# Kernel optimization log

Measured on AMD Instinct MI355X. Metric: run time of the kernel, lower is better.

Reference implementation:

```python
import jax, jax.numpy as jnp
import numpy as np

N = 100000
E = 1600000
EPS = 1e-5

def setup_inputs() -> dict:
    key = jax.random.key(0)
    ks = jax.random.split(key, 10)
    d_in, d_h, d_out = 128, 128, 64
    sc = lambda d: 1.0 / np.sqrt(d)
    return {
        "x": jax.random.normal(ks[0], (N, d_in), jnp.float32),
        "edge_src": jax.random.randint(ks[1], (E,), 0, N, jnp.int32),
        "edge_dst": jax.random.randint(ks[2], (E,), 0, N, jnp.int32),
        "Wr0": jax.random.normal(ks[3], (d_in, d_h), jnp.float32) * sc(d_in),
        "Wn0": jax.random.normal(ks[4], (d_in, d_h), jnp.float32) * sc(d_in),
        "b0": jnp.zeros((d_h,), jnp.float32),
        "g0": jnp.ones((d_h,), jnp.float32),
        "be0": jnp.zeros((d_h,), jnp.float32),
        "Wr1": jax.random.normal(ks[5], (d_h, d_h), jnp.float32) * sc(d_h),
        "Wn1": jax.random.normal(ks[6], (d_h, d_h), jnp.float32) * sc(d_h),
        "b1": jnp.zeros((d_h,), jnp.float32),
        "g1": jnp.ones((d_h,), jnp.float32),
        "be1": jnp.zeros((d_h,), jnp.float32),
        "Wr2": jax.random.normal(ks[7], (d_h, d_out), jnp.float32) * sc(d_h),
        "Wn2": jax.random.normal(ks[8], (d_h, d_out), jnp.float32) * sc(d_h),
        "b2": jnp.zeros((d_out,), jnp.float32),
    }

def _mean_agg(x, src, dst):
    # GraphSAGE mean aggregation: scatter-mean of source features onto dst nodes
    deg = jax.ops.segment_sum(jnp.ones((src.shape[0],), x.dtype), dst, num_segments=N)
    s = jax.ops.segment_sum(x[src], dst, num_segments=N)  # [N, d] gather+scatter
    return s / jnp.maximum(deg, 1.0)[:, None]

def _sage_conv(x, src, dst, Wr, Wn, b):
    return x @ Wr + _mean_agg(x, src, dst) @ Wn + b

def _layernorm(h, g, b):
    mu = h.mean(-1, keepdims=True)
    var = ((h - mu) ** 2).mean(-1, keepdims=True)
    return (h - mu) * jax.lax.rsqrt(var + EPS) * g + b

def reference(x, edge_src, edge_dst, Wr0, Wn0, b0, g0, be0,
              Wr1, Wn1, b1, g1, be1, Wr2, Wn2, b2):
    # layer 0: conv -> dropout(eval=identity) -> LayerNorm -> relu
    h = _sage_conv(x, edge_src, edge_dst, Wr0, Wn0, b0)
    h = jax.nn.relu(_layernorm(h, g0, be0))
    # layer 1
    h = _sage_conv(h, edge_src, edge_dst, Wr1, Wn1, b1)
    h = jax.nn.relu(_layernorm(h, g1, be1))
    # final conv + log_softmax over classes
    h = _sage_conv(h, edge_src, edge_dst, Wr2, Wn2, b2)
    return jax.nn.log_softmax(h, axis=1)
```

## Files before the change

kernel.cpp:

```cpp
#include <hip/hip_runtime.h>
#include <math.h>

#define N_NODES 100000
#define NPAD 100032
#define N_EDGES 1600000
#define EPS 1e-5f
#define NC 256
#define CHUNK 6250
#define NR 98
#define RSZ 1024
#define NRC (NR * NC)

typedef __bf16 bf16x8 __attribute__((ext_vector_type(8)));
typedef float f32x4 __attribute__((ext_vector_type(4)));
typedef float f32x2 __attribute__((ext_vector_type(2)));

__device__ inline unsigned short f2bf(float f) {
    unsigned u = __float_as_uint(f);
    unsigned r = u + 0x7fffu + ((u >> 16) & 1u);
    return (unsigned short)(r >> 16);
}
__device__ inline float bflo(unsigned u) { return __uint_as_float(u << 16); }
__device__ inline float bfhi(unsigned u) { return __uint_as_float(u & 0xffff0000u); }
__device__ inline unsigned pack2(float lo, float hi) {
    return (unsigned)f2bf(lo) | ((unsigned)f2bf(hi) << 16);
}
__device__ inline unsigned char f2fp8(float f) {
    return (unsigned char)(__builtin_amdgcn_cvt_pk_fp8_f32(f, f, 0, false) & 0xff);
}

__global__ __launch_bounds__(256) void k_prep(const float* __restrict__ x,
                                              unsigned short* __restrict__ xb,
                                              unsigned* __restrict__ xq8,
                                              const int* __restrict__ dst,
                                              int* __restrict__ cntG) {
    __shared__ int hist[NR];
    int t = threadIdx.x;
    if (blockIdx.x < 12500) {
        int idx = blockIdx.x * 256 + t;
        float4 v = ((const float4*)x)[idx];
        ushort4 o;
        o.x = f2bf(v.x); o.y = f2bf(v.y); o.z = f2bf(v.z); o.w = f2bf(v.w);
        ((ushort4*)xb)[idx] = o;
        int q = __builtin_amdgcn_cvt_pk_fp8_f32(v.x, v.y, 0, false);
        q = __builtin_amdgcn_cvt_pk_fp8_f32(v.z, v.w, q, true);
        xq8[idx] = (unsigned)q;
    } else {
        int c = blockIdx.x - 12500;
        for (int i = t; i < NR; i += 256) hist[i] = 0;
        __syncthreads();
        int base = c * CHUNK;
        for (int i = base + t; i < base + CHUNK; i += 256)
            atomicAdd(&hist[dst[i] >> 10], 1);
        __syncthreads();
        for (int i = t; i < NR; i += 256) cntG[i * NC + c] = hist[i];
    }
}

__global__ __launch_bounds__(256) void k_scanA_prepw(
        int* __restrict__ cntG,
        const float* __restrict__ Wr0, const float* __restrict__ Wn0,
        const float* __restrict__ Wr1, const float* __restrict__ Wn1,
        const float* __restrict__ Wr2, const float* __restrict__ Wn2,
        unsigned short* __restrict__ WT0, unsigned short* __restrict__ WT1,
        unsigned short* __restrict__ WT2) {
    int t = threadIdx.x;
    if (blockIdx.x == 0) {
        __shared__ int ts[256];
        const int PER = NRC / 256;
        int s = 0;
        for (int i = 0; i < PER; ++i) s += cntG[t * PER + i];
        ts[t] = s;
        __syncthreads();
        #pragma unroll
        for (int off = 1; off < 256; off <<= 1) {
            int y = 0;
            if (t >= off) y = ts[t - off];
            __syncthreads();
            if (t >= off) ts[t] += y;
            __syncthreads();
        }
        int run = ts[t] - s;
        for (int i = 0; i < PER; ++i) {
            int v = cntG[t * PER + i];
            cntG[t * PER + i] = run;
            run += v;
        }
    } else {
        int b = blockIdx.x - 1;
        if (b < 256) {
            const float* Wr = (b < 128) ? Wr0 : Wr1;
            const float* Wn = (b < 128) ? Wn0 : Wn1;
            unsigned short* WT = (b < 128) ? WT0 : WT1;
            int idx = (b & 127) * 256 + t;
            int n = idx >> 8;
            int kc = idx & 255;
            float v = (kc < 128) ? Wr[kc * 128 + n] : Wn[(kc - 128) * 128 + n];
            WT[idx] = f2bf(v);
        } else {
            int idx = (b - 256) * 256 + t;
            int n = idx >> 7;
            int k = idx & 127;
            float v = (n < 64) ? Wr2[k * 64 + n] : Wn2[k * 64 + (n - 64)];
            WT2[n * 128 + k] = f2bf(v);
        }
    }
}

__global__ __launch_bounds__(1024) void k_bin(const int* __restrict__ src,
                                              const int* __restrict__ dst,
                                              const int* __restrict__ baseG,
                                              unsigned* __restrict__ bpack) {
    __shared__ int cur[NR];
    int t = threadIdx.x, c = blockIdx.x;
    for (int i = t; i < NR; i += 1024) cur[i] = baseG[i * NC + c];
    __syncthreads();
    int base = c * CHUNK;
    for (int i = base + t; i < base + CHUNK; i += 1024) {
        int d = dst[i];
        unsigned s = (unsigned)src[i];
        int p = atomicAdd(&cur[d >> 10], 1);
        bpack[p] = (s << 10) | (unsigned)(d & 1023);
    }
}

__global__ __launch_bounds__(1024) void k_nodeplace(
        const unsigned* __restrict__ bpack, const int* __restrict__ baseG,
        int* __restrict__ deg, float* __restrict__ invdeg,
        int* __restrict__ rowptr, int* __restrict__ eidx) {
    __shared__ int hist[RSZ];
    __shared__ int cur[RSZ];
    __shared__ int wbase[16];
    int r = blockIdx.x, t = threadIdx.x;
    hist[t] = 0;
    __syncthreads();
    int s0 = baseG[r * NC];
    int s1 = (r == NR - 1) ? N_EDGES : baseG[(r + 1) * NC];
    int nbase = r << 10;
    for (int i = s0 + t; i < s1; i += 1024)
        atomicAdd(&hist[bpack[i] & 1023u], 1);
    __syncthreads();
    int lane = t & 63, wv = t >> 6;
    int d = hist[t];
    int s = d;
    #pragma unroll
    for (int m = 1; m < 64; m <<= 1) {
        int y = __shfl_up(s, m);
        if (lane >= m) s += y;
    }
    if (lane == 63) wbase[wv] = s;
    __syncthreads();
    if (t < 16) {
        int v = wbase[t];
        int sv = v;
        #pragma unroll
        for (int m = 1; m < 16; m <<= 1) {
            int y = __shfl_up(sv, m);
            if (t >= m) sv += y;
        }
        wbase[t] = sv - v;
    }
    __syncthreads();
    int p = s0 + wbase[wv] + s - d;
    cur[t] = p;
    int n = nbase + t;
    if (n < N_NODES) {
        rowptr[n] = p;
        deg[n] = d;
        invdeg[n] = 1.0f / fmaxf((float)d, 1.0f);
    }
    __syncthreads();
    for (int i = s0 + t; i < s1; i += 1024) {
        unsigned bp = bpack[i];
        int pp = atomicAdd(&cur[bp & 1023u], 1);
        eidx[pp] = (int)(bp >> 10);
    }
}

__global__ __launch_bounds__(256) void k_gather(const uint4* __restrict__ hq4,
                                                const int* __restrict__ eidx,
                                                const int* __restrict__ rowptr,
                                                const int* __restrict__ deg,
                                                const float* __restrict__ invdeg,
                                                uint4* __restrict__ aggw4) {
    int node = blockIdx.x * 32 + (threadIdx.x >> 3);
    int l = threadIdx.x & 7;
    int start = rowptr[node];
    int cnt = deg[node];
    f32x2 a[8];
    #pragma unroll
    for (int i = 0; i < 8; ++i) a[i] = (f32x2)0.0f;

    auto accum = [&](uint4 u) {
        a[0] += __builtin_amdgcn_cvt_pk_f32_fp8((int)u.x, false);
        a[1] += __builtin_amdgcn_cvt_pk_f32_fp8((int)u.x, true);
        a[2] += __builtin_amdgcn_cvt_pk_f32_fp8((int)u.y, false);
        a[3] += __builtin_amdgcn_cvt_pk_f32_fp8((int)u.y, true);
        a[4] += __builtin_amdgcn_cvt_pk_f32_fp8((int)u.z, false);
        a[5] += __builtin_amdgcn_cvt_pk_f32_fp8((int)u.z, true);
        a[6] += __builtin_amdgcn_cvt_pk_f32_fp8((int)u.w, false);
        a[7] += __builtin_amdgcn_cvt_pk_f32_fp8((int)u.w, true);
    };

    int j = 0;
    for (; j + 4 <= cnt; j += 4) {
        int s0 = eidx[start + j];
        int s1 = eidx[start + j + 1];
        int s2 = eidx[start + j + 2];
        int s3 = eidx[start + j + 3];
        uint4 u0 = hq4[(size_t)s0 * 8 + l];
        uint4 u1 = hq4[(size_t)s1 * 8 + l];
        uint4 u2 = hq4[(size_t)s2 * 8 + l];
        uint4 u3 = hq4[(size_t)s3 * 8 + l];
        accum(u0); accum(u1); accum(u2); accum(u3);
    }
    for (; j < cnt; ++j) {
        uint4 u = hq4[(size_t)eidx[start + j] * 8 + l];
        accum(u);
    }

    float id = invdeg[node];
    uint4 o0, o1;
    o0.x = pack2(a[0].x * id, a[0].y * id);
    o0.y = pack2(a[1].x * id, a[1].y * id);
    o0.z = pack2(a[2].x * id, a[2].y * id);
    o0.w = pack2(a[3].x * id, a[3].y * id);
    o1.x = pack2(a[4].x * id, a[4].y * id);
    o1.y = pack2(a[5].x * id, a[5].y * id);
    o1.z = pack2(a[6].x * id, a[6].y * id);
    o1.w = pack2(a[7].x * id, a[7].y * id);
    aggw4[(size_t)node * 16 + l * 2] = o0;
    aggw4[(size_t)node * 16 + l * 2 + 1] = o1;
}

__global__ __launch_bounds__(512) void k_gemm_ln(
        const unsigned short* __restrict__ hb, const unsigned short* __restrict__ ab,
        const unsigned short* __restrict__ WT,
        const float* __restrict__ b, const float* __restrict__ g,
        const float* __restrict__ be, unsigned short* __restrict__ outb,
        unsigned char* __restrict__ outq8) {
    __shared__ unsigned short hl[64][136];
    __shared__ unsigned short al[64][136];
    __shared__ unsigned short bt[128][72];
    __shared__ float p1[2][64], p2[2][64];

    const int tid = threadIdx.x;
    const int lane = tid & 63;
    const int w = tid >> 6;
    const int quad = lane >> 4;
    const int l15 = lane & 15;
    const int rt = w >> 1;
    const int ch = w & 1;
    const int row0 = blockIdx.x * 64;

    #pragma unroll
    for (int t = 0; t < 2; ++t) {
        int idx = tid + t * 512;
        int r = idx >> 4;
        int c8 = idx & 15;
        *(float4*)&hl[r][c8 * 8] = ((const float4*)hb)[(size_t)(row0 + r) * 16 + c8];
        *(float4*)&al[r][c8 * 8] = ((const float4*)ab)[(size_t)(row0 + r) * 16 + c8];
    }

    f32x4 acc[4];
    #pragma unroll
    for (int t = 0; t < 4; ++t)
        #pragma unroll
        for (int r = 0; r < 4; ++r) acc[t][r] = 0.0f;

    #pragma unroll
    for (int kt = 0; kt < 4; ++kt) {
        __syncthreads();
        #pragma unroll
        for (int t = 0; t < 2; ++t) {
            int idx = tid + t * 512;
            int n = idx >> 3;
            int c8 = idx & 7;
            *(float4*)&bt[n][c8 * 8] = ((const float4*)WT)[n * 32 + kt * 8 + c8];
        }
        __syncthreads();
        #pragma unroll
        for (int ks = 0; ks < 2; ++ks) {
            const int ck = kt * 64 + ks * 32;
            const unsigned short* ap = (ck < 128)
                ? &hl[rt * 16 + l15][ck + quad * 8]
                : &al[rt * 16 + l15][ck - 128 + quad * 8];
            bf16x8 a = *(const bf16x8*)ap;
            #pragma unroll
            for (int t = 0; t < 4; ++t) {
                bf16x8 bb = *(const bf16x8*)&bt[ch * 64 + t * 16 + l15][ks * 32 + quad * 8];
                acc[t] = __builtin_amdgcn_mfma_f32_16x16x32_bf16(a, bb, acc[t], 0, 0, 0);
            }
        }
    }

    float bcol[4], gc[4], bec[4];
    #pragma unroll
    for (int t = 0; t < 4; ++t) {
        int col = ch * 64 + t * 16 + l15;
        bcol[t] = b[col]; gc[t] = g[col]; bec[t] = be[col];
    }
    float v[4][4];
    float s1[4], s2[4];
    #pragma unroll
    for (int r = 0; r < 4; ++r) { s1[r] = 0.0f; s2[r] = 0.0f; }
    #pragma unroll
    for (int t = 0; t < 4; ++t)
        #pragma unroll
        for (int r = 0; r < 4; ++r) {
            float x = acc[t][r] + bcol[t];
            v[t][r] = x;
            s1[r] += x;
            s2[r] += x * x;
        }
    #pragma unroll
    for (int m = 1; m <= 8; m <<= 1)
        #pragma unroll
        for (int r = 0; r < 4; ++r) {
            s1[r] += __shfl_xor(s1[r], m);
            s2[r] += __shfl_xor(s2[r], m);
        }
    if (l15 == 0) {
        #pragma unroll
        for (int r = 0; r < 4; ++r) {
            int rl = rt * 16 + quad * 4 + r;
            p1[ch][rl] = s1[r];
            p2[ch][rl] = s2[r];
        }
    }
    __syncthreads();
    #pragma unroll
    for (int r = 0; r < 4; ++r) {
        int rl = rt * 16 + quad * 4 + r;
        float S1 = p1[0][rl] + p1[1][rl];
        float S2 = p2[0][rl] + p2[1][rl];
        float mean = S1 * (1.0f / 128.0f);
        float var = S2 * (1.0f / 128.0f) - mean * mean;
        float rstd = rsqrtf(var + EPS);
        #pragma unroll
        for (int t = 0; t < 4; ++t) {
            int col = ch * 64 + t * 16 + l15;
            float o = fmaxf((v[t][r] - mean) * rstd * gc[t] + bec[t], 0.0f);
            outb[(size_t)(row0 + rl) * 128 + col] = f2bf(o);
            if (outq8) outq8[(size_t)(row0 + rl) * 128 + col] = f2fp8(o);
        }
    }
}

__global__ __launch_bounds__(512) void k_gemm2(
        const unsigned short* __restrict__ hb, const unsigned short* __restrict__ WT,
        const float* __restrict__ b2, unsigned short* __restrict__ zb16,
        unsigned char* __restrict__ yq8) {
    __shared__ unsigned short hl[64][136];
    __shared__ unsigned short bt[128][136];

    const int tid = threadIdx.x;
    const int lane = tid & 63;
    const int w = tid >> 6;
    const int quad = lane >> 4;
    const int l15 = lane & 15;
    const int rt = w >> 1;
    const int ch = w & 1;
    const int row0 = blockIdx.x * 64;

    #pragma unroll
    for (int t = 0; t < 2; ++t) {
        int idx = tid + t * 512;
        int r = idx >> 4;
        int c8 = idx & 15;
        *(float4*)&hl[r][c8 * 8] = ((const float4*)hb)[(size_t)(row0 + r) * 16 + c8];
    }
    #pragma unroll
    for (int t = 0; t < 4; ++t) {
        int idx = tid + t * 512;
        int n = idx >> 4;
        int c8 = idx & 15;
        *(float4*)&bt[n][c8 * 8] = ((const float4*)WT)[n * 16 + c8];
    }
    __syncthreads();

    f32x4 acc[4];
    #pragma unroll
    for (int t = 0; t < 4; ++t)
        #pragma unroll
        for (int r = 0; r < 4; ++r) acc[t][r] = 0.0f;

    #pragma unroll
    for (int ks = 0; ks < 4; ++ks) {
        bf16x8 a = *(const bf16x8*)&hl[rt * 16 + l15][ks * 32 + quad * 8];
        #pragma unroll
        for (int t = 0; t < 4; ++t) {
            bf16x8 bb = *(const bf16x8*)&bt[ch * 64 + t * 16 + l15][ks * 32 + quad * 8];
            acc[t] = __builtin_amdgcn_mfma_f32_16x16x32_bf16(a, bb, acc[t], 0, 0, 0);
        }
    }

    if (ch == 0) {
        #pragma unroll
        for (int t = 0; t < 4; ++t) {
            int col = t * 16 + l15;
            float bc = b2[col];
            #pragma unroll
            for (int r = 0; r < 4; ++r) {
                int rl = rt * 16 + quad * 4 + r;
                zb16[(size_t)(row0 + rl) * 64 + col] = f2bf(acc[t][r] + bc);
            }
        }
    } else {
        #pragma unroll
        for (int t = 0; t < 4; ++t) {
            int col = t * 16 + l15;
            #pragma unroll
            for (int r = 0; r < 4; ++r) {
                int rl = rt * 16 + quad * 4 + r;
                yq8[(size_t)(row0 + rl) * 64 + col] = f2fp8(acc[t][r]);
            }
        }
    }
}

__global__ __launch_bounds__(256) void k_l2g(const uint4* __restrict__ yq4,
                                             const unsigned short* __restrict__ zb16,
                                             const int* __restrict__ eidx,
                                             const int* __restrict__ rowptr,
                                             const int* __restrict__ deg,
                                             const float* __restrict__ invdeg,
                                             float* __restrict__ out) {
    int node = blockIdx.x * 64 + (threadIdx.x >> 2);
    if (node >= N_NODES) return;
    int l = threadIdx.x & 3;
    int start = rowptr[node];
    int cnt = deg[node];
    f32x2 a[8];
    #pragma unroll
    for (int i = 0; i < 8; ++i) a[i] = (f32x2)0.0f;

    auto accum = [&](uint4 u) {
        a[0] += __builtin_amdgcn_cvt_pk_f32_fp8((int)u.x, false);
        a[1] += __builtin_amdgcn_cvt_pk_f32_fp8((int)u.x, true);
        a[2] += __builtin_amdgcn_cvt_pk_f32_fp8((int)u.y, false);
        a[3] += __builtin_amdgcn_cvt_pk_f32_fp8((int)u.y, true);
        a[4] += __builtin_amdgcn_cvt_pk_f32_fp8((int)u.z, false);
        a[5] += __builtin_amdgcn_cvt_pk_f32_fp8((int)u.z, true);
        a[6] += __builtin_amdgcn_cvt_pk_f32_fp8((int)u.w, false);
        a[7] += __builtin_amdgcn_cvt_pk_f32_fp8((int)u.w, true);
    };

    int j = 0;
    for (; j + 4 <= cnt; j += 4) {
        int s0 = eidx[start + j];
        int s1 = eidx[start + j + 1];
        int s2 = eidx[start + j + 2];
        int s3 = eidx[start + j + 3];
        uint4 u0 = yq4[(size_t)s0 * 4 + l];
        uint4 u1 = yq4[(size_t)s1 * 4 + l];
        uint4 u2 = yq4[(size_t)s2 * 4 + l];
        uint4 u3 = yq4[(size_t)s3 * 4 + l];
        accum(u0); accum(u1); accum(u2); accum(u3);
    }
    for (; j < cnt; ++j) {
        uint4 u = yq4[(size_t)eidx[start + j] * 4 + l];
        accum(u);
    }

    float id = invdeg[node];
    uint4 z0 = ((const uint4*)zb16)[(size_t)node * 8 + l * 2];
    uint4 z1 = ((const uint4*)zb16)[(size_t)node * 8 + l * 2 + 1];
    float v[16];
    v[0]  = bflo(z0.x) + a[0].x * id; v[1]  = bfhi(z0.x) + a[0].y * id;
    v[2]  = bflo(z0.y) + a[1].x * id; v[3]  = bfhi(z0.y) + a[1].y * id;
    v[4]  = bflo(z0.z) + a[2].x * id; v[5]  = bfhi(z0.z) + a[2].y * id;
    v[6]  = bflo(z0.w) + a[3].x * id; v[7]  = bfhi(z0.w) + a[3].y * id;
    v[8]  = bflo(z1.x) + a[4].x * id; v[9]  = bfhi(z1.x) + a[4].y * id;
    v[10] = bflo(z1.y) + a[5].x * id; v[11] = bfhi(z1.y) + a[5].y * id;
    v[12] = bflo(z1.z) + a[6].x * id; v[13] = bfhi(z1.z) + a[6].y * id;
    v[14] = bflo(z1.w) + a[7].x * id; v[15] = bfhi(z1.w) + a[7].y * id;

    float m = v[0];
    #pragma unroll
    for (int i = 1; i < 16; ++i) m = fmaxf(m, v[i]);
    m = fmaxf(m, __shfl_xor(m, 1));
    m = fmaxf(m, __shfl_xor(m, 2));
    float s = 0.0f;
    #pragma unroll
    for (int i = 0; i < 16; ++i) s += __expf(v[i] - m);
    s += __shfl_xor(s, 1);
    s += __shfl_xor(s, 2);
    float L = m + logf(s);
    #pragma unroll
    for (int k = 0; k < 4; ++k) {
        float4 o;
        o.x = v[4 * k] - L; o.y = v[4 * k + 1] - L;
        o.z = v[4 * k + 2] - L; o.w = v[4 * k + 3] - L;
        ((float4*)out)[(size_t)node * 16 + l * 4 + k] = o;
    }
}

extern "C" void kernel_launch(void* const* d_in, const int* in_sizes, int n_in,
                              void* d_out, int out_size, void* d_ws, size_t ws_size,
                              hipStream_t stream) {
    const float* x   = (const float*)d_in[0];
    const int* esrc  = (const int*)d_in[1];
    const int* edst  = (const int*)d_in[2];
    const float* Wr0 = (const float*)d_in[3];
    const float* Wn0 = (const float*)d_in[4];
    const float* b0  = (const float*)d_in[5];
    const float* g0  = (const float*)d_in[6];
    const float* be0 = (const float*)d_in[7];
    const float* Wr1 = (const float*)d_in[8];
    const float* Wn1 = (const float*)d_in[9];
    const float* b1  = (const float*)d_in[10];
    const float* g1  = (const float*)d_in[11];
    const float* be1 = (const float*)d_in[12];
    const float* Wr2 = (const float*)d_in[13];
    const float* Wn2 = (const float*)d_in[14];
    const float* b2  = (const float*)d_in[15];
    float* out = (float*)d_out;

    char* p = (char*)d_ws;
    auto alloc = [&](size_t bytes) {
        void* r = (void*)p;
        p += (bytes + 255) & ~(size_t)255;
        return r;
    };
    int*   deg    = (int*)  alloc(N_NODES * 4);
    float* invdeg = (float*)alloc(N_NODES * 4);
    int*   rowptr = (int*)  alloc(N_NODES * 4);
    int*   cntG   = (int*)  alloc(NRC * 4);
    unsigned* bpack = (unsigned*)alloc((size_t)N_EDGES * 4);
    int*   eidx   = (int*)  alloc((size_t)N_EDGES * 4);
    unsigned short* xb   = (unsigned short*)alloc((size_t)NPAD * 128 * 2);
    unsigned short* h1   = (unsigned short*)alloc((size_t)NPAD * 128 * 2);
    unsigned short* aggb = (unsigned short*)alloc((size_t)NPAD * 128 * 2);
    unsigned*       xq8  = (unsigned*)      alloc((size_t)N_NODES * 128);
    unsigned char*  h1q8 = (unsigned char*) alloc((size_t)NPAD * 128);
    unsigned short* zb16 = (unsigned short*)alloc((size_t)NPAD * 64 * 2);
    unsigned char*  yq8  = (unsigned char*) alloc((size_t)NPAD * 64);
    unsigned short* WT0  = (unsigned short*)alloc(128 * 256 * 2);
    unsigned short* WT1  = (unsigned short*)alloc(128 * 256 * 2);
    unsigned short* WT2  = (unsigned short*)alloc(128 * 128 * 2);

    k_prep<<<12500 + NC, 256, 0, stream>>>(x, xb, xq8, edst, cntG);
    k_scanA_prepw<<<321, 256, 0, stream>>>(cntG, Wr0, Wn0, Wr1, Wn1, Wr2, Wn2,
                                           WT0, WT1, WT2);
    k_bin<<<NC, 1024, 0, stream>>>(esrc, edst, cntG, bpack);
    k_nodeplace<<<NR, 1024, 0, stream>>>(bpack, cntG, deg, invdeg, rowptr, eidx);

    k_gather<<<N_NODES / 32, 256, 0, stream>>>((const uint4*)xq8, eidx, rowptr, deg, invdeg, (uint4*)aggb);
    k_gemm_ln<<<NPAD / 64, 512, 0, stream>>>(xb, aggb, WT0, b0, g0, be0, h1, h1q8);

    k_gather<<<N_NODES / 32, 256, 0, stream>>>((const uint4*)h1q8, eidx, rowptr, deg, invdeg, (uint4*)aggb);
    k_gemm_ln<<<NPAD / 64, 512, 0, stream>>>(h1, aggb, WT1, b1, g1, be1, xb, (unsigned char*)nullptr);

    k_gemm2<<<NPAD / 64, 512, 0, stream>>>(xb, WT2, b2, zb16, yq8);
    k_l2g<<<(N_NODES + 63) / 64, 256, 0, stream>>>((const uint4*)yq8, zb16, eidx, rowptr, deg, invdeg, out);
}
```

Baseline: 353.4 us.

## Fuse neighbor mean-gather into the GEMM+LayerNorm kernel prologue

Removes the separate k_gather kernel and computes each 64-row tile's mean-aggregated neighbor features directly into shared memory inside k_gemm_ln. This drops the bf16 aggregation buffer's write and read round trip through global memory, plus two kernel launches. In exchange the GEMM blocks must wait on irregular gather latency before doing any math. The launch bounds now request higher occupancy (512 threads, 4 blocks), which may limit registers.

```diff
diff --git a/kernel.cpp b/kernel.cpp
--- a/kernel.cpp
+++ b/kernel.cpp
@@ -177,64 +177,11 @@
     }
 }
 
-__global__ __launch_bounds__(256) void k_gather(const uint4* __restrict__ hq4,
-                                                const int* __restrict__ eidx,
-                                                const int* __restrict__ rowptr,
-                                                const int* __restrict__ deg,
-                                                const float* __restrict__ invdeg,
-                                                uint4* __restrict__ aggw4) {
-    int node = blockIdx.x * 32 + (threadIdx.x >> 3);
-    int l = threadIdx.x & 7;
-    int start = rowptr[node];
-    int cnt = deg[node];
-    f32x2 a[8];
-    #pragma unroll
-    for (int i = 0; i < 8; ++i) a[i] = (f32x2)0.0f;
-
-    auto accum = [&](uint4 u) {
-        a[0] += __builtin_amdgcn_cvt_pk_f32_fp8((int)u.x, false);
-        a[1] += __builtin_amdgcn_cvt_pk_f32_fp8((int)u.x, true);
-        a[2] += __builtin_amdgcn_cvt_pk_f32_fp8((int)u.y, false);
-        a[3] += __builtin_amdgcn_cvt_pk_f32_fp8((int)u.y, true);
-        a[4] += __builtin_amdgcn_cvt_pk_f32_fp8((int)u.z, false);
-        a[5] += __builtin_amdgcn_cvt_pk_f32_fp8((int)u.z, true);
-        a[6] += __builtin_amdgcn_cvt_pk_f32_fp8((int)u.w, false);
-        a[7] += __builtin_amdgcn_cvt_pk_f32_fp8((int)u.w, true);
-    };
-
-    int j = 0;
-    for (; j + 4 <= cnt; j += 4) {
-        int s0 = eidx[start + j];
-        int s1 = eidx[start + j + 1];
-        int s2 = eidx[start + j + 2];
-        int s3 = eidx[start + j + 3];
-        uint4 u0 = hq4[(size_t)s0 * 8 + l];
-        uint4 u1 = hq4[(size_t)s1 * 8 + l];
-        uint4 u2 = hq4[(size_t)s2 * 8 + l];
-        uint4 u3 = hq4[(size_t)s3 * 8 + l];
-        accum(u0); accum(u1); accum(u2); accum(u3);
-    }
-    for (; j < cnt; ++j) {
-        uint4 u = hq4[(size_t)eidx[start + j] * 8 + l];
-        accum(u);
-    }
-
-    float id = invdeg[node];
-    uint4 o0, o1;
-    o0.x = pack2(a[0].x * id, a[0].y * id);
-    o0.y = pack2(a[1].x * id, a[1].y * id);
-    o0.z = pack2(a[2].x * id, a[2].y * id);
-    o0.w = pack2(a[3].x * id, a[3].y * id);
-    o1.x = pack2(a[4].x * id, a[4].y * id);
-    o1.y = pack2(a[5].x * id, a[5].y * id);
-    o1.z = pack2(a[6].x * id, a[6].y * id);
-    o1.w = pack2(a[7].x * id, a[7].y * id);
-    aggw4[(size_t)node * 16 + l * 2] = o0;
-    aggw4[(size_t)node * 16 + l * 2 + 1] = o1;
-}
-
-__global__ __launch_bounds__(512) void k_gemm_ln(
-        const unsigned short* __restrict__ hb, const unsigned short* __restrict__ ab,
+__global__ __launch_bounds__(512, 4) void k_gemm_ln(
+        const unsigned short* __restrict__ hb,
+        const uint4* __restrict__ hq4,
+        const int* __restrict__ eidx, const int* __restrict__ rowptr,
+        const int* __restrict__ deg, const float* __restrict__ invdeg,
         const unsigned short* __restrict__ WT,
         const float* __restrict__ b, const float* __restrict__ g,
         const float* __restrict__ be, unsigned short* __restrict__ outb,
@@ -259,7 +206,57 @@
         int r = idx >> 4;
         int c8 = idx & 15;
         *(float4*)&hl[r][c8 * 8] = ((const float4*)hb)[(size_t)(row0 + r) * 16 + c8];
-        *(float4*)&al[r][c8 * 8] = ((const float4*)ab)[(size_t)(row0 + r) * 16 + c8];
+    }
+
+    {
+        int r = tid >> 3;
+        int l = tid & 7;
+        int node = row0 + r;
+        uint4 o0 = {0, 0, 0, 0}, o1 = {0, 0, 0, 0};
+        if (node < N_NODES) {
+            int start = rowptr[node];
+            int cnt = deg[node];
+            f32x2 a[8];
+            #pragma unroll
+            for (int i = 0; i < 8; ++i) a[i] = (f32x2)0.0f;
+            auto accum = [&](uint4 u) {
+                a[0] += __builtin_amdgcn_cvt_pk_f32_fp8((int)u.x, false);
+                a[1] += __builtin_amdgcn_cvt_pk_f32_fp8((int)u.x, true);
+                a[2] += __builtin_amdgcn_cvt_pk_f32_fp8((int)u.y, false);
+                a[3] += __builtin_amdgcn_cvt_pk_f32_fp8((int)u.y, true);
+                a[4] += __builtin_amdgcn_cvt_pk_f32_fp8((int)u.z, false);
+                a[5] += __builtin_amdgcn_cvt_pk_f32_fp8((int)u.z, true);
+                a[6] += __builtin_amdgcn_cvt_pk_f32_fp8((int)u.w, false);
+                a[7] += __builtin_amdgcn_cvt_pk_f32_fp8((int)u.w, true);
+            };
+            int j = 0;
+            for (; j + 4 <= cnt; j += 4) {
+                int s0 = eidx[start + j];
+                int s1 = eidx[start + j + 1];
+                int s2 = eidx[start + j + 2];
+                int s3 = eidx[start + j + 3];
+                uint4 u0 = hq4[(size_t)s0 * 8 + l];
+                uint4 u1 = hq4[(size_t)s1 * 8 + l];
+                uint4 u2 = hq4[(size_t)s2 * 8 + l];
+                uint4 u3 = hq4[(size_t)s3 * 8 + l];
+                accum(u0); accum(u1); accum(u2); accum(u3);
+            }
+            for (; j < cnt; ++j) {
+                uint4 u = hq4[(size_t)eidx[start + j] * 8 + l];
+                accum(u);
+            }
+            float id = invdeg[node];
+            o0.x = pack2(a[0].x * id, a[0].y * id);
+            o0.y = pack2(a[1].x * id, a[1].y * id);
+            o0.z = pack2(a[2].x * id, a[2].y * id);
+            o0.w = pack2(a[3].x * id, a[3].y * id);
+            o1.x = pack2(a[4].x * id, a[4].y * id);
+            o1.y = pack2(a[5].x * id, a[5].y * id);
+            o1.z = pack2(a[6].x * id, a[6].y * id);
+            o1.w = pack2(a[7].x * id, a[7].y * id);
+        }
+        *(uint4*)&al[r][l * 16] = o0;
+        *(uint4*)&al[r][l * 16 + 8] = o1;
     }
 
     f32x4 acc[4];
@@ -531,7 +528,6 @@
     int*   eidx   = (int*)  alloc((size_t)N_EDGES * 4);
     unsigned short* xb   = (unsigned short*)alloc((size_t)NPAD * 128 * 2);
     unsigned short* h1   = (unsigned short*)alloc((size_t)NPAD * 128 * 2);
-    unsigned short* aggb = (unsigned short*)alloc((size_t)NPAD * 128 * 2);
     unsigned*       xq8  = (unsigned*)      alloc((size_t)N_NODES * 128);
     unsigned char*  h1q8 = (unsigned char*) alloc((size_t)NPAD * 128);
     unsigned short* zb16 = (unsigned short*)alloc((size_t)NPAD * 64 * 2);
@@ -546,11 +542,12 @@
     k_bin<<<NC, 1024, 0, stream>>>(esrc, edst, cntG, bpack);
     k_nodeplace<<<NR, 1024, 0, stream>>>(bpack, cntG, deg, invdeg, rowptr, eidx);
 
-    k_gather<<<N_NODES / 32, 256, 0, stream>>>((const uint4*)xq8, eidx, rowptr, deg, invdeg, (uint4*)aggb);
-    k_gemm_ln<<<NPAD / 64, 512, 0, stream>>>(xb, aggb, WT0, b0, g0, be0, h1, h1q8);
-
-    k_gather<<<N_NODES / 32, 256, 0, stream>>>((const uint4*)h1q8, eidx, rowptr, deg, invdeg, (uint4*)aggb);
-    k_gemm_ln<<<NPAD / 64, 512, 0, stream>>>(h1, aggb, WT1, b1, g1, be1, xb, (unsigned char*)nullptr);
+    k_gemm_ln<<<NPAD / 64, 512, 0, stream>>>(xb, (const uint4*)xq8, eidx, rowptr,
+                                             deg, invdeg, WT0, b0, g0, be0, h1, h1q8);
+
+    k_gemm_ln<<<NPAD / 64, 512, 0, stream>>>(h1, (const uint4*)h1q8, eidx, rowptr,
+                                             deg, invdeg, WT1, b1, g1, be1, xb,
+                                             (unsigned char*)nullptr);
 
     k_gemm2<<<NPAD / 64, 512, 0, stream>>>(xb, WT2, b2, zb16, yq8);
     k_l2g<<<(N_NODES + 63) / 64, 256, 0, stream>>>((const uint4*)yq8, zb16, eidx, rowptr, deg, invdeg, out);
```

Measured after the change: 350.2 us. No clear change (-0.9%).
